# Performance work log

Measured on AMD Instinct MI355X. Metric: run time of the kernel, lower is better.

The kernel has to match this reference:

```python
import jax, jax.numpy as jnp
import numpy as np

B, T_IN, T_OUT = 256, 256, 256
D_IN, HID, OUT = 512, 1024, 1024


def _lstm_step(carry, x_t, W, b):
    # W: [d_x + d_h, 4*d_h] stacked gates (input, forget, output, candidate)
    h, c = carry
    gates = jnp.concatenate([x_t, h], axis=1) @ W + b  # [B, 4*d_h]
    i, f, o, g = jnp.split(gates, 4, axis=1)
    i, f, o = jax.nn.sigmoid(i), jax.nn.sigmoid(f), jax.nn.sigmoid(o)
    g = jnp.tanh(g)
    c_next = f * c + i * g
    h_next = o * jnp.tanh(c_next)
    return (h_next, c_next)


def setup_inputs() -> dict:
    key = jax.random.key(0)
    ks = jax.random.split(key, 9)
    def lin(k, fan_in, fan_out):
        return jax.random.normal(k, (fan_in, fan_out), dtype=jnp.float32) / np.sqrt(fan_in)
    x = jax.random.normal(ks[0], (B, T_IN, D_IN), dtype=jnp.float32)
    enc_W = lin(ks[1], D_IN + HID, 4 * HID)
    enc_b = jnp.zeros((4 * HID,), jnp.float32)
    dec_W = lin(ks[2], HID + OUT, 4 * OUT)
    dec_b = jnp.zeros((4 * OUT,), jnp.float32)
    Wh = lin(ks[3], HID, OUT)
    bh = jnp.zeros((OUT,), jnp.float32)
    Wc = lin(ks[4], HID, OUT)
    bc = jnp.zeros((OUT,), jnp.float32)
    return {"x": x, "enc_W": enc_W, "enc_b": enc_b, "dec_W": dec_W,
            "dec_b": dec_b, "Wh": Wh, "bh": bh, "Wc": Wc, "bc": bc}


def reference(x, enc_W, enc_b, dec_W, dec_b, Wh, bh, Wc, bc):
    Bm = x.shape[0]
    # ---- encoder: scan over time ----
    h0 = jnp.zeros((Bm, HID), x.dtype)
    c0 = jnp.zeros((Bm, HID), x.dtype)
    def enc_step(carry, x_t):
        return _lstm_step(carry, x_t, enc_W, enc_b), None
    (h_enc, c_enc), _ = jax.lax.scan(enc_step, (h0, c0), jnp.swapaxes(x, 0, 1))
    # ---- decoder: constant input = h_enc, init projected states ----
    h_cur = h_enc @ Wh + bh
    c_cur = c_enc @ Wc + bc
    def dec_step(carry, _):
        nxt = _lstm_step(carry, h_enc, dec_W, dec_b)
        return nxt, nxt[0]
    _, hs = jax.lax.scan(dec_step, (h_cur, c_cur), None, length=T_OUT)
    return jnp.swapaxes(hs, 0, 1)  # [B, T_OUT, OUT]
```

## Files before the change

kernel.cpp:

```cpp
#include <hip/hip_runtime.h>
#include <hip/hip_bf16.h>


#define NB   256
#define TSEQ 256
#define DIN  512
#define HID  1024
#define G4   4096

typedef __attribute__((ext_vector_type(8))) __bf16 bf16x8;
typedef __attribute__((ext_vector_type(4))) float  f32x4;

static __device__ __forceinline__ unsigned short f2bf(float v) {
    unsigned u; __builtin_memcpy(&u, &v, 4);
    return (unsigned short)((u + 0x7FFFu + ((u >> 16) & 1u)) >> 16);
}
static __device__ __forceinline__ float bf2f(unsigned short b) {
    unsigned u = ((unsigned)b) << 16; float f; __builtin_memcpy(&f, &u, 4); return f;
}
static __device__ __forceinline__ float fsig(float x) {
    return 1.f / (1.f + __expf(-x));
}
static __device__ __forceinline__ float ftanh(float x) {
    return 2.f / (1.f + __expf(-2.f * x)) - 1.f;
}
template<int AUX>
static __device__ __forceinline__ void glds16(const void* g, void* l) {
    __builtin_amdgcn_global_load_lds(
        (const __attribute__((address_space(1))) unsigned int*)g,
        (__attribute__((address_space(3))) unsigned int*)l, 16, 0, AUX);
}
static __device__ __forceinline__ void st16_ag(unsigned short* p, unsigned short v) {
    asm volatile("global_store_short %0, %1, off sc1"
                 :: "v"(p), "v"((unsigned)v) : "memory");
}
static __device__ __forceinline__ void st32_ag(unsigned* p, unsigned v) {
    asm volatile("global_store_dword %0, %1, off sc1"
                 :: "v"(p), "v"(v) : "memory");
}

__global__ __launch_bounds__(256) void split_transpose(
        const float* __restrict__ W, unsigned short* __restrict__ T_hi,
        unsigned short* __restrict__ T_lo, int K, int N) {
    __shared__ float tile[64][65];
    const int kb = blockIdx.x * 64, nb = blockIdx.y * 64;
    const int tid = threadIdx.x;
    const int r = tid >> 2, c0 = (tid & 3) << 4;
    #pragma unroll
    for (int j = 0; j < 16; j += 4) {
        float4 v = *(const float4*)(W + (size_t)(kb + r) * N + nb + c0 + j);
        tile[r][c0 + j + 0] = v.x; tile[r][c0 + j + 1] = v.y;
        tile[r][c0 + j + 2] = v.z; tile[r][c0 + j + 3] = v.w;
    }
    __syncthreads();
    #pragma unroll
    for (int j = 0; j < 16; ++j) {
        float v = tile[c0 + j][r];
        unsigned short hi = f2bf(v);
        unsigned short lo = f2bf(v - bf2f(hi));
        size_t o = (size_t)(nb + r) * K + kb + c0 + j;
        T_hi[o] = hi; T_lo[o] = lo;
    }
}

__global__ __launch_bounds__(256, 1) void lstm_persist(
        const float* __restrict__ x,
        const unsigned short* __restrict__ encT_hi, const unsigned short* __restrict__ encT_lo,
        const unsigned short* __restrict__ decT_hi, const unsigned short* __restrict__ decT_lo,
        const unsigned short* __restrict__ WhT_hi, const unsigned short* __restrict__ WhT_lo,
        const unsigned short* __restrict__ WcT_hi, const unsigned short* __restrict__ WcT_lo,
        const float* __restrict__ enc_b, const float* __restrict__ dec_b,
        const float* __restrict__ bhv, const float* __restrict__ bcv,
        unsigned short* h_hi0, unsigned short* h_lo0,
        unsigned short* h_hi1, unsigned short* h_lo1,
        unsigned short* ce_hi, unsigned short* ce_lo,
        float* c0, float* c1,
        unsigned short* x_hi0, unsigned short* x_lo0,
        unsigned short* x_hi1, unsigned short* x_lo1,
        unsigned* barcnt, float* __restrict__ out) {
    __shared__ __align__(16) char smem[131072];
    __shared__ float sG[64][68];
    const int wg   = blockIdx.x;
    const int row0 = (wg >> 6) << 6;
    const int hc0  = (wg & 63) << 4;
    const int tid  = threadIdx.x;
    const int lane = tid & 63;
    const int wv   = tid >> 6;
    const int rA   = (wv >> 1) << 5;
    const int cB   = (wv & 1) << 5;
    const int n    = tid & 15, mq = tid >> 4;

    unsigned bar_e = 0;
    auto gbar = [&]() {
        __syncthreads();
        ++bar_e;
        if (tid == 0) {
            __hip_atomic_fetch_add(barcnt + ((wg & 7) << 5), 1u,
                                   __ATOMIC_RELAXED, __HIP_MEMORY_SCOPE_AGENT);
            if (wg == 0) {
                const unsigned target = bar_e << 8;
                for (;;) {
                    unsigned s = 0;
                    #pragma unroll
                    for (int i = 0; i < 8; ++i)
                        s += __hip_atomic_load(barcnt + (i << 5),
                                               __ATOMIC_RELAXED, __HIP_MEMORY_SCOPE_AGENT);
                    if (s >= target) break;
                    __builtin_amdgcn_s_sleep(1);
                }
                __hip_atomic_fetch_add(barcnt + 256, 1u,
                                       __ATOMIC_RELAXED, __HIP_MEMORY_SCOPE_AGENT);
            } else {
                while (__hip_atomic_load(barcnt + 256,
                                         __ATOMIC_RELAXED, __HIP_MEMORY_SCOPE_AGENT) < bar_e)
                    __builtin_amdgcn_s_sleep(2);
            }
        }
        __syncthreads();
    };

    const unsigned short *g_Axh = nullptr, *g_Axl = nullptr;
    const unsigned short *g_Ahh = nullptr, *g_Ahl = nullptr;
    const unsigned short *g_Bh = nullptr, *g_Bl = nullptr;
    int g_sb = 0, g_kb0 = 0, g_nx = 0, g_colw0 = 0, g_arow0 = 0;

    auto stageB = [&](int c, int buf) {
        char* bb = smem + buf * 32768;
        const int k0b = g_kb0 + (c << 6);
        const int kseg = (lane & 7) ^ ((lane >> 3) & 7);
        #pragma unroll
        for (int j = 0; j < 2; ++j) {
            const int colw = g_colw0 + (j << 3) + (lane >> 3);
            const size_t go = (size_t)colw * g_sb + k0b + (kseg << 3);
            const int gclb = (wv << 4) + (j << 3);
            glds16<0>(g_Bh + go, bb + 16384 + (gclb << 7));
            glds16<0>(g_Bl + go, bb + 24576 + (gclb << 7));
        }
    };
    auto stageA = [&](int c, int buf) {
        char* bb = smem + buf * 32768;
        const int kseg = (lane & 7) ^ ((lane >> 3) & 7);
        const unsigned short *Ah, *Al; int sa, ka;
        if (c < g_nx) { Ah = g_Axh; Al = g_Axl; sa = DIN; ka = c << 6; }
        else          { Ah = g_Ahh; Al = g_Ahl; sa = HID; ka = (c - g_nx) << 6; }
        #pragma unroll
        for (int j = 0; j < 2; ++j) {
            const int mb2 = (wv << 4) + (j << 3);
            const int m   = mb2 + (lane >> 3);
            const size_t go = (size_t)(g_arow0 + m) * sa + ka + (kseg << 3);
            glds16<16>(Ah + go, bb + (mb2 << 7));
            glds16<16>(Al + go, bb + 8192 + (mb2 << 7));
        }
    };

    auto compute = [&](const char* bb, f32x4 (&acc)[2][2]) {
        const char* sah = bb;
        const char* sal = bb + 8192;
        const char* sbh = bb + 16384;
        const char* sbl = bb + 24576;
        #pragma unroll
        for (int kk = 0; kk < 2; ++kk) {
            const int kb = (kk << 6) | ((lane >> 4) << 4);
            bf16x8 ah[2], al[2], bh[2], bl[2];
            #pragma unroll
            for (int ms = 0; ms < 2; ++ms) {
                const int m  = rA + (ms << 4) + (lane & 15);
                const int ad = (m << 7) + (kb ^ ((m & 7) << 4));
                ah[ms] = *(const bf16x8*)(sah + ad);
                al[ms] = *(const bf16x8*)(sal + ad);
            }
            #pragma unroll
            for (int ns = 0; ns < 2; ++ns) {
                const int gcl = cB + (ns << 4) + (lane & 15);
                const int ad  = (gcl << 7) + (kb ^ ((gcl & 7) << 4));
                bh[ns] = *(const bf16x8*)(sbh + ad);
                bl[ns] = *(const bf16x8*)(sbl + ad);
            }
            #pragma unroll
            for (int ms = 0; ms < 2; ++ms)
                #pragma unroll
                for (int ns = 0; ns < 2; ++ns) {
                    acc[ms][ns] = __builtin_amdgcn_mfma_f32_16x16x32_bf16(ah[ms], bh[ns], acc[ms][ns], 0, 0, 0);
                    acc[ms][ns] = __builtin_amdgcn_mfma_f32_16x16x32_bf16(al[ms], bh[ns], acc[ms][ns], 0, 0, 0);
                    acc[ms][ns] = __builtin_amdgcn_mfma_f32_16x16x32_bf16(ah[ms], bl[ns], acc[ms][ns], 0, 0, 0);
                }
        }
    };

    auto run_chunks = [&](int nch, f32x4 (&acc)[2][2], int preB) {
        if (!preB) { stageB(0, 0); stageA(0, 0); stageB(1, 1); stageA(1, 1); }
        else       { stageA(0, 0); stageA(1, 1); }
        for (int c = 0; c < nch; ++c) {
            if (c + 2 < nch) {
                stageB(c + 2, (c + 2) & 3);
                stageA(c + 2, (c + 2) & 3);
                if (preB && c == 0)
                    asm volatile("s_waitcnt vmcnt(12)" ::: "memory");
                else
                    asm volatile("s_waitcnt vmcnt(16)" ::: "memory");
            } else if (c + 1 < nch) {
                asm volatile("s_waitcnt vmcnt(8)" ::: "memory");
            } else {
                asm volatile("s_waitcnt vmcnt(0)" ::: "memory");
            }
            __builtin_amdgcn_s_barrier();
            compute(smem + (c & 3) * 32768, acc);
        }
    };

    auto acc2sG = [&](f32x4 (&acc)[2][2]) {
        #pragma unroll
        for (int ms = 0; ms < 2; ++ms)
            #pragma unroll
            for (int ns = 0; ns < 2; ++ns)
                #pragma unroll
                for (int r = 0; r < 4; ++r)
                    sG[cB + (ns << 4) + (lane & 15)]
                      [rA + (ms << 4) + ((lane >> 4) << 2) + r] = acc[ms][ns][r];
    };

    auto convert = [&](int tn) {
        unsigned short* xh = (tn & 1) ? x_hi1 : x_hi0;
        unsigned short* xl = (tn & 1) ? x_lo1 : x_lo0;
        const int r = tid & 63, cp = tid >> 6;
        const int row = row0 + r;
        const int col = ((wg & 63) << 3) + (cp << 1);
        const unsigned long long pv = __builtin_nontemporal_load(
            (const unsigned long long*)(x + ((size_t)row * TSEQ + tn) * DIN + col));
        const float fx = __uint_as_float((unsigned)pv);
        const float fy = __uint_as_float((unsigned)(pv >> 32));
        const unsigned short hx = f2bf(fx), lx = f2bf(fx - bf2f(hx));
        const unsigned short hy = f2bf(fy), ly = f2bf(fy - bf2f(hy));
        st32_ag((unsigned*)(xh + (size_t)row * DIN + col), (unsigned)hx | ((unsigned)hy << 16));
        st32_ag((unsigned*)(xl + (size_t)row * DIN + col), (unsigned)lx | ((unsigned)ly << 16));
    };

    const float be0 = enc_b[hc0 + n];
    const float be1 = enc_b[HID + hc0 + n];
    const float be2 = enc_b[2 * HID + hc0 + n];
    const float be3 = enc_b[3 * HID + hc0 + n];

    g_Bh = encT_hi; g_Bl = encT_lo; g_sb = 1536; g_kb0 = 0; g_nx = 8;
    g_colw0 = wv * HID + hc0; g_arow0 = row0;
    convert(0);
    stageB(0, 0); stageB(1, 1);
    gbar();
    for (int t = 0; t < TSEQ; ++t) {
        g_Axh = (t & 1) ? x_hi1 : x_hi0;  g_Axl = (t & 1) ? x_lo1 : x_lo0;
        g_Ahh = (t & 1) ? h_hi1 : h_hi0;  g_Ahl = (t & 1) ? h_lo1 : h_lo0;
        unsigned short* Ohh = (t & 1) ? h_hi0 : h_hi1;
        unsigned short* Ohl = (t & 1) ? h_lo0 : h_lo1;
        f32x4 acc[2][2];
        { f32x4 z; z[0]=0.f;z[1]=0.f;z[2]=0.f;z[3]=0.f;
          acc[0][0]=z;acc[0][1]=z;acc[1][0]=z;acc[1][1]=z; }
        run_chunks(24, acc, 1);
        acc2sG(acc);
        __syncthreads();
        #pragma unroll
        for (int q = 0; q < 4; ++q) {
            const int m = mq + (q << 4);
            const int grow = row0 + m;
            const float gi = sG[n][m] + be0;
            const float gf = sG[16 + n][m] + be1;
            const float go = sG[32 + n][m] + be2;
            const float gg = sG[48 + n][m] + be3;
            const float si = fsig(gi), sf = fsig(gf), so = fsig(go);
            const float tg = ftanh(gg);
            const size_t ci = (size_t)grow * HID + hc0 + n;
            const float cnew = sf * c0[ci] + si * tg;
            c0[ci] = cnew;
            const float hnew = so * ftanh(cnew);
            const unsigned short hh = f2bf(hnew);
            st16_ag(Ohh + ci, hh);
            st16_ag(Ohl + ci, f2bf(hnew - bf2f(hh)));
            if (t == TSEQ - 1) {
                const unsigned short ch = f2bf(cnew);
                st16_ag(ce_hi + ci, ch);
                st16_ag(ce_lo + ci, f2bf(cnew - bf2f(ch)));
            }
        }
        if (t < TSEQ - 1) {
            convert(t + 1);
            stageB(0, 0); stageB(1, 1);
        }
        gbar();
    }

    float dk[16];
    {
        g_Bh = decT_hi; g_Bl = decT_lo; g_sb = 2048; g_kb0 = 0; g_nx = 0;
        g_Ahh = h_hi0; g_Ahl = h_lo0;
        g_colw0 = wv * HID + hc0; g_arow0 = row0;
        f32x4 acc[2][2];
        { f32x4 z; z[0]=0.f;z[1]=0.f;z[2]=0.f;z[3]=0.f;
          acc[0][0]=z;acc[0][1]=z;acc[1][0]=z;acc[1][1]=z; }
        run_chunks(16, acc, 0);
        acc2sG(acc);
        __syncthreads();
        #pragma unroll
        for (int q = 0; q < 4; ++q) {
            const int m = mq + (q << 4);
            dk[q * 4 + 0] = sG[n][m]      + dec_b[hc0 + n];
            dk[q * 4 + 1] = sG[16 + n][m] + dec_b[HID + hc0 + n];
            dk[q * 4 + 2] = sG[32 + n][m] + dec_b[2 * HID + hc0 + n];
            dk[q * 4 + 3] = sG[48 + n][m] + dec_b[3 * HID + hc0 + n];
        }
        gbar();
    }

    if (wg < 128) {
        const int isWc = wg >> 6;
        const int wgl  = wg & 63;
        const int mgp = wgl >> 4, ngp = wgl & 15;
        g_arow0 = mgp << 6;
        g_colw0 = (ngp << 6) + (wv << 4);
        g_Bh = isWc ? WcT_hi : WhT_hi;  g_Bl = isWc ? WcT_lo : WhT_lo;
        g_sb = 1024; g_kb0 = 0; g_nx = 0;
        g_Ahh = isWc ? ce_hi : h_hi0;   g_Ahl = isWc ? ce_lo : h_lo0;
        f32x4 acc[2][2];
        { f32x4 z; z[0]=0.f;z[1]=0.f;z[2]=0.f;z[3]=0.f;
          acc[0][0]=z;acc[0][1]=z;acc[1][0]=z;acc[1][1]=z; }
        run_chunks(16, acc, 0);
        #pragma unroll
        for (int ms = 0; ms < 2; ++ms)
            #pragma unroll
            for (int ns = 0; ns < 2; ++ns)
                #pragma unroll
                for (int r = 0; r < 4; ++r) {
                    const int rowp = (mgp << 6) + rA + (ms << 4) + ((lane >> 4) << 2) + r;
                    const int colp = (ngp << 6) + cB + (ns << 4) + (lane & 15);
                    const size_t o = (size_t)rowp * HID + colp;
                    if (isWc) {
                        st32_ag((unsigned*)(c1 + o),
                                __float_as_uint(acc[ms][ns][r] + bcv[colp]));
                    } else {
                        const float v = acc[ms][ns][r] + bhv[colp];
                        const unsigned short hh = f2bf(v);
                        st16_ag(h_hi1 + o, hh);
                        st16_ag(h_lo1 + o, f2bf(v - bf2f(hh)));
                    }
                }
    }
    gbar();

    g_Bh = decT_hi; g_Bl = decT_lo; g_sb = 2048; g_kb0 = 1024; g_nx = 0;
    g_colw0 = wv * HID + hc0; g_arow0 = row0;
    float creg[4];
    #pragma unroll
    for (int q = 0; q < 4; ++q) {
        const size_t ci = (size_t)(row0 + mq + (q << 4)) * HID + hc0 + n;
        creg[q] = __uint_as_float(__hip_atomic_load((const unsigned*)(c1 + ci),
                      __ATOMIC_RELAXED, __HIP_MEMORY_SCOPE_AGENT));
    }
    stageB(0, 0); stageB(1, 1);
    for (int t = 0; t < TSEQ; ++t) {
        g_Ahh = (t & 1) ? h_hi0 : h_hi1;  g_Ahl = (t & 1) ? h_lo0 : h_lo1;
        unsigned short* Ohh = (t & 1) ? h_hi1 : h_hi0;
        unsigned short* Ohl = (t & 1) ? h_lo1 : h_lo0;
        f32x4 acc[2][2];
        { f32x4 z; z[0]=0.f;z[1]=0.f;z[2]=0.f;z[3]=0.f;
          acc[0][0]=z;acc[0][1]=z;acc[1][0]=z;acc[1][1]=z; }
        run_chunks(16, acc, 1);
        acc2sG(acc);
        __syncthreads();
        #pragma unroll
        for (int q = 0; q < 4; ++q) {
            const int m = mq + (q << 4);
            const int grow = row0 + m;
            const float gi = sG[n][m]      + dk[q * 4 + 0];
            const float gf = sG[16 + n][m] + dk[q * 4 + 1];
            const float go = sG[32 + n][m] + dk[q * 4 + 2];
            const float gg = sG[48 + n][m] + dk[q * 4 + 3];
            const float si = fsig(gi), sf = fsig(gf), so = fsig(go);
            const float tg = ftanh(gg);
            const float cnew = sf * creg[q] + si * tg;
            creg[q] = cnew;
            const float hnew = so * ftanh(cnew);
            const size_t ci = (size_t)grow * HID + hc0 + n;
            const unsigned short hh = f2bf(hnew);
            st16_ag(Ohh + ci, hh);
            st16_ag(Ohl + ci, f2bf(hnew - bf2f(hh)));
            __builtin_nontemporal_store(hnew,
                out + ((size_t)grow * TSEQ + t) * HID + hc0 + n);
        }
        if (t < TSEQ - 1) {
            stageB(0, 0); stageB(1, 1);
            gbar();
        }
    }
}

extern "C" void kernel_launch(void* const* d_in, const int* in_sizes, int n_in,
                              void* d_out, int out_size, void* d_ws, size_t ws_size,
                              hipStream_t stream) {
    (void)in_sizes; (void)n_in; (void)out_size;
    const float* x     = (const float*)d_in[0];
    const float* enc_W = (const float*)d_in[1];
    const float* enc_b = (const float*)d_in[2];
    const float* dec_W = (const float*)d_in[3];
    const float* dec_b = (const float*)d_in[4];
    const float* Wh    = (const float*)d_in[5];
    const float* bh    = (const float*)d_in[6];
    const float* Wc    = (const float*)d_in[7];
    const float* bc    = (const float*)d_in[8];
    float* out = (float*)d_out;

    char* w = (char*)d_ws;
    size_t off = 0;
    auto alloc = [&](size_t bytes) -> void* {
        off = (off + 255) & ~(size_t)255;
        void* p = w + off;
        off += bytes;
        return p;
    };
    unsigned short* encT_hi = (unsigned short*)alloc((size_t)G4 * 1536 * 2);
    unsigned short* encT_lo = (unsigned short*)alloc((size_t)G4 * 1536 * 2);
    unsigned short* decT_hi = (unsigned short*)alloc((size_t)G4 * 2048 * 2);
    unsigned short* decT_lo = (unsigned short*)alloc((size_t)G4 * 2048 * 2);
    unsigned short* WhT_hi  = (unsigned short*)alloc((size_t)HID * HID * 2);
    unsigned short* WhT_lo  = (unsigned short*)alloc((size_t)HID * HID * 2);
    unsigned short* WcT_hi  = (unsigned short*)alloc((size_t)HID * HID * 2);
    unsigned short* WcT_lo  = (unsigned short*)alloc((size_t)HID * HID * 2);
    unsigned short* h_hi0 = (unsigned short*)alloc((size_t)NB * HID * 2);
    unsigned short* h_lo0 = (unsigned short*)alloc((size_t)NB * HID * 2);
    unsigned short* h_hi1 = (unsigned short*)alloc((size_t)NB * HID * 2);
    unsigned short* h_lo1 = (unsigned short*)alloc((size_t)NB * HID * 2);
    unsigned short* ce_hi = (unsigned short*)alloc((size_t)NB * HID * 2);
    unsigned short* ce_lo = (unsigned short*)alloc((size_t)NB * HID * 2);
    float* c0 = (float*)alloc((size_t)NB * HID * 4);
    float* c1 = (float*)alloc((size_t)NB * HID * 4);
    unsigned short* x_hi0 = (unsigned short*)alloc((size_t)NB * DIN * 2);
    unsigned short* x_lo0 = (unsigned short*)alloc((size_t)NB * DIN * 2);
    unsigned short* x_hi1 = (unsigned short*)alloc((size_t)NB * DIN * 2);
    unsigned short* x_lo1 = (unsigned short*)alloc((size_t)NB * DIN * 2);
    unsigned* barcnt = (unsigned*)alloc(2048);
    if (off > ws_size) return;

    split_transpose<<<dim3(1536 / 64, G4 / 64), 256, 0, stream>>>(enc_W, encT_hi, encT_lo, 1536, G4);
    split_transpose<<<dim3(2048 / 64, G4 / 64), 256, 0, stream>>>(dec_W, decT_hi, decT_lo, 2048, G4);
    split_transpose<<<dim3(HID / 64, HID / 64), 256, 0, stream>>>(Wh, WhT_hi, WhT_lo, HID, HID);
    split_transpose<<<dim3(HID / 64, HID / 64), 256, 0, stream>>>(Wc, WcT_hi, WcT_lo, HID, HID);
    (void)hipMemsetAsync(h_hi0, 0, (size_t)NB * HID * 2, stream);
    (void)hipMemsetAsync(h_lo0, 0, (size_t)NB * HID * 2, stream);
    (void)hipMemsetAsync(c0,    0, (size_t)NB * HID * 4, stream);
    (void)hipMemsetAsync(barcnt, 0, 2048, stream);

    lstm_persist<<<256, 256, 0, stream>>>(
        x, encT_hi, encT_lo, decT_hi, decT_lo, WhT_hi, WhT_lo, WcT_hi, WcT_lo,
        enc_b, dec_b, bh, bc,
        h_hi0, h_lo0, h_hi1, h_lo1, ce_hi, ce_lo, c0, c1,
        x_hi0, x_lo0, x_hi1, x_lo1, barcnt, out);
}
```

Baseline: 10.59 ms.

## Load A operand via registers with deeper prefetch pipeline instead of direct-to-LDS

```diff
diff --git a/kernel.cpp b/kernel.cpp
--- a/kernel.cpp
+++ b/kernel.cpp
@@ -10,6 +10,9 @@
 
 typedef __attribute__((ext_vector_type(8))) __bf16 bf16x8;
 typedef __attribute__((ext_vector_type(4))) float  f32x4;
+typedef unsigned long long ull;
+
+struct alignas(16) ull2 { ull a, b; };
 
 static __device__ __forceinline__ unsigned short f2bf(float v) {
     unsigned u; __builtin_memcpy(&u, &v, 4);
@@ -24,11 +27,10 @@
 static __device__ __forceinline__ float ftanh(float x) {
     return 2.f / (1.f + __expf(-2.f * x)) - 1.f;
 }
-template<int AUX>
 static __device__ __forceinline__ void glds16(const void* g, void* l) {
     __builtin_amdgcn_global_load_lds(
         (const __attribute__((address_space(1))) unsigned int*)g,
-        (__attribute__((address_space(3))) unsigned int*)l, 16, 0, AUX);
+        (__attribute__((address_space(3))) unsigned int*)l, 16, 0, 0);
 }
 static __device__ __forceinline__ void st16_ag(unsigned short* p, unsigned short v) {
     asm volatile("global_store_short %0, %1, off sc1"
@@ -78,7 +80,7 @@
         unsigned short* x_hi0, unsigned short* x_lo0,
         unsigned short* x_hi1, unsigned short* x_lo1,
         unsigned* barcnt, float* __restrict__ out) {
-    __shared__ __align__(16) char smem[131072];
+    __shared__ __align__(16) char smem[98304];
     __shared__ float sG[64][68];
     const int wg   = blockIdx.x;
     const int row0 = (wg >> 6) << 6;
@@ -125,7 +127,7 @@
     int g_sb = 0, g_kb0 = 0, g_nx = 0, g_colw0 = 0, g_arow0 = 0;
 
     auto stageB = [&](int c, int buf) {
-        char* bb = smem + buf * 32768;
+        char* bb = smem + 32768 + buf * 16384;
         const int k0b = g_kb0 + (c << 6);
         const int kseg = (lane & 7) ^ ((lane >> 3) & 7);
         #pragma unroll
@@ -133,31 +135,44 @@
             const int colw = g_colw0 + (j << 3) + (lane >> 3);
             const size_t go = (size_t)colw * g_sb + k0b + (kseg << 3);
             const int gclb = (wv << 4) + (j << 3);
-            glds16<0>(g_Bh + go, bb + 16384 + (gclb << 7));
-            glds16<0>(g_Bl + go, bb + 24576 + (gclb << 7));
-        }
-    };
-    auto stageA = [&](int c, int buf) {
-        char* bb = smem + buf * 32768;
-        const int kseg = (lane & 7) ^ ((lane >> 3) & 7);
+            glds16(g_Bh + go, bb + (gclb << 7));
+            glds16(g_Bl + go, bb + 8192 + (gclb << 7));
+        }
+    };
+
+    auto aload = [&](int ch, ull (&r)[8]) {
         const unsigned short *Ah, *Al; int sa, ka;
-        if (c < g_nx) { Ah = g_Axh; Al = g_Axl; sa = DIN; ka = c << 6; }
-        else          { Ah = g_Ahh; Al = g_Ahl; sa = HID; ka = (c - g_nx) << 6; }
-        #pragma unroll
-        for (int j = 0; j < 2; ++j) {
-            const int mb2 = (wv << 4) + (j << 3);
-            const int m   = mb2 + (lane >> 3);
-            const size_t go = (size_t)(g_arow0 + m) * sa + ka + (kseg << 3);
-            glds16<16>(Ah + go, bb + (mb2 << 7));
-            glds16<16>(Al + go, bb + 8192 + (mb2 << 7));
-        }
-    };
-
-    auto compute = [&](const char* bb, f32x4 (&acc)[2][2]) {
-        const char* sah = bb;
-        const char* sal = bb + 8192;
-        const char* sbh = bb + 16384;
-        const char* sbl = bb + 24576;
+        if (ch < g_nx) { Ah = g_Axh; Al = g_Axl; sa = DIN; ka = ch << 6; }
+        else           { Ah = g_Ahh; Al = g_Ahl; sa = HID; ka = (ch - g_nx) << 6; }
+        const int qa = tid & 3, mA = tid >> 2;
+        const ull* ph = (const ull*)(Ah + (size_t)(g_arow0 + mA) * sa + ka + (qa << 4));
+        const ull* pl = (const ull*)(Al + (size_t)(g_arow0 + mA) * sa + ka + (qa << 4));
+        #pragma unroll
+        for (int i = 0; i < 4; ++i)
+            r[i] = __hip_atomic_load(ph + i, __ATOMIC_RELAXED, __HIP_MEMORY_SCOPE_AGENT);
+        #pragma unroll
+        for (int i = 0; i < 4; ++i)
+            r[4 + i] = __hip_atomic_load(pl + i, __ATOMIC_RELAXED, __HIP_MEMORY_SCOPE_AGENT);
+    };
+    auto dswrite = [&](int ch, const ull (&r)[8]) {
+        char* ab = smem + (ch & 1) * 16384;
+        const int qa = tid & 3, mA = tid >> 2;
+        const int base = mA << 7, sw = mA & 7;
+        const int o0 = base + ((((qa << 1) + 0) ^ sw) << 4);
+        const int o1 = base + ((((qa << 1) + 1) ^ sw) << 4);
+        *(ull2*)(ab + o0)        = ull2{r[0], r[1]};
+        *(ull2*)(ab + o1)        = ull2{r[2], r[3]};
+        *(ull2*)(ab + 8192 + o0) = ull2{r[4], r[5]};
+        *(ull2*)(ab + 8192 + o1) = ull2{r[6], r[7]};
+    };
+
+    auto compute = [&](int c, f32x4 (&acc)[2][2]) {
+        const char* ab  = smem + (c & 1) * 16384;
+        const char* bbf = smem + 32768 + (c & 3) * 16384;
+        const char* sah = ab;
+        const char* sal = ab + 8192;
+        const char* sbh = bbf;
+        const char* sbl = bbf + 8192;
         #pragma unroll
         for (int kk = 0; kk < 2; ++kk) {
             const int kb = (kk << 6) | ((lane >> 4) << 4);
@@ -187,24 +202,43 @@
         }
     };
 
-    auto run_chunks = [&](int nch, f32x4 (&acc)[2][2], int preB) {
-        if (!preB) { stageB(0, 0); stageA(0, 0); stageB(1, 1); stageA(1, 1); }
-        else       { stageA(0, 0); stageA(1, 1); }
-        for (int c = 0; c < nch; ++c) {
-            if (c + 2 < nch) {
-                stageB(c + 2, (c + 2) & 3);
-                stageA(c + 2, (c + 2) & 3);
-                if (preB && c == 0)
-                    asm volatile("s_waitcnt vmcnt(12)" ::: "memory");
-                else
-                    asm volatile("s_waitcnt vmcnt(16)" ::: "memory");
-            } else if (c + 1 < nch) {
-                asm volatile("s_waitcnt vmcnt(8)" ::: "memory");
-            } else {
-                asm volatile("s_waitcnt vmcnt(0)" ::: "memory");
-            }
-            __builtin_amdgcn_s_barrier();
-            compute(smem + (c & 3) * 32768, acc);
+    auto vwait = [&](int nw) {
+        if (nw >= 32)      asm volatile("s_waitcnt vmcnt(32)" ::: "memory");
+        else if (nw == 24) asm volatile("s_waitcnt vmcnt(24)" ::: "memory");
+        else if (nw == 16) asm volatile("s_waitcnt vmcnt(16)" ::: "memory");
+        else if (nw == 4)  asm volatile("s_waitcnt vmcnt(4)"  ::: "memory");
+        else               asm volatile("s_waitcnt vmcnt(0)"  ::: "memory");
+    };
+
+    auto body = [&](int c, int nch, ull (&sw)[8], f32x4 (&acc)[2][2]) {
+        int nw;
+        if (c == 0) nw = 16;
+        else if (c == 1) nw = 24;
+        else {
+            const int rem = nch - 1 - c;
+            nw = (rem >= 4) ? 32 : (rem == 3) ? 24 : (rem == 2) ? 16 : (rem == 1) ? 4 : 0;
+        }
+        vwait(nw);
+        asm volatile("s_waitcnt lgkmcnt(0)" ::: "memory");
+        __builtin_amdgcn_s_barrier();
+        if (c + 1 < nch) dswrite(c + 1, sw);
+        if (c + 3 < nch) stageB(c + 3, (c + 3) & 3);
+        if (c + 5 < nch) aload(c + 5, sw);
+        compute(c, acc);
+    };
+
+    auto run_chunks = [&](int nch, f32x4 (&acc)[2][2]) {
+        ull r0[8], r1[8], r2[8], r3[8];
+        aload(0, r0); aload(1, r1); aload(2, r2); aload(3, r3);
+        stageB(0, 0); stageB(1, 1); stageB(2, 2);
+        asm volatile("s_waitcnt vmcnt(36)" ::: "memory");
+        dswrite(0, r0);
+        aload(4, r0);
+        for (int cb = 0; cb < nch; cb += 4) {
+            body(cb + 0, nch, r1, acc);
+            body(cb + 1, nch, r2, acc);
+            body(cb + 2, nch, r3, acc);
+            body(cb + 3, nch, r0, acc);
         }
     };
 
@@ -225,8 +259,8 @@
         const int r = tid & 63, cp = tid >> 6;
         const int row = row0 + r;
         const int col = ((wg & 63) << 3) + (cp << 1);
-        const unsigned long long pv = __builtin_nontemporal_load(
-            (const unsigned long long*)(x + ((size_t)row * TSEQ + tn) * DIN + col));
+        const ull pv = __builtin_nontemporal_load(
+            (const ull*)(x + ((size_t)row * TSEQ + tn) * DIN + col));
         const float fx = __uint_as_float((unsigned)pv);
         const float fy = __uint_as_float((unsigned)(pv >> 32));
         const unsigned short hx = f2bf(fx), lx = f2bf(fx - bf2f(hx));
@@ -243,7 +277,6 @@
     g_Bh = encT_hi; g_Bl = encT_lo; g_sb = 1536; g_kb0 = 0; g_nx = 8;
     g_colw0 = wv * HID + hc0; g_arow0 = row0;
     convert(0);
-    stageB(0, 0); stageB(1, 1);
     gbar();
     for (int t = 0; t < TSEQ; ++t) {
         g_Axh = (t & 1) ? x_hi1 : x_hi0;  g_Axl = (t & 1) ? x_lo1 : x_lo0;
@@ -253,7 +286,7 @@
         f32x4 acc[2][2];
         { f32x4 z; z[0]=0.f;z[1]=0.f;z[2]=0.f;z[3]=0.f;
           acc[0][0]=z;acc[0][1]=z;acc[1][0]=z;acc[1][1]=z; }
-        run_chunks(24, acc, 1);
+        run_chunks(24, acc);
         acc2sG(acc);
         __syncthreads();
         #pragma unroll
@@ -279,10 +312,7 @@
                 st16_ag(ce_lo + ci, f2bf(cnew - bf2f(ch)));
             }
         }
-        if (t < TSEQ - 1) {
-            convert(t + 1);
-            stageB(0, 0); stageB(1, 1);
-        }
+        if (t < TSEQ - 1) convert(t + 1);
         gbar();
     }
 
@@ -294,7 +324,7 @@
         f32x4 acc[2][2];
         { f32x4 z; z[0]=0.f;z[1]=0.f;z[2]=0.f;z[3]=0.f;
           acc[0][0]=z;acc[0][1]=z;acc[1][0]=z;acc[1][1]=z; }
-        run_chunks(16, acc, 0);
+        run_chunks(16, acc);
         acc2sG(acc);
         __syncthreads();
         #pragma unroll
@@ -320,7 +350,7 @@
         f32x4 acc[2][2];
         { f32x4 z; z[0]=0.f;z[1]=0.f;z[2]=0.f;z[3]=0.f;
           acc[0][0]=z;acc[0][1]=z;acc[1][0]=z;acc[1][1]=z; }
-        run_chunks(16, acc, 0);
+        run_chunks(16, acc);
         #pragma unroll
         for (int ms = 0; ms < 2; ++ms)
             #pragma unroll
@@ -352,7 +382,7 @@
         creg[q] = __uint_as_float(__hip_atomic_load((const unsigned*)(c1 + ci),
                       __ATOMIC_RELAXED, __HIP_MEMORY_SCOPE_AGENT));
     }
-    stageB(0, 0); stageB(1, 1);
+    asm volatile("s_waitcnt vmcnt(0)" ::: "memory");
     for (int t = 0; t < TSEQ; ++t) {
         g_Ahh = (t & 1) ? h_hi0 : h_hi1;  g_Ahl = (t & 1) ? h_lo0 : h_lo1;
         unsigned short* Ohh = (t & 1) ? h_hi1 : h_hi0;
@@ -360,7 +390,7 @@
         f32x4 acc[2][2];
         { f32x4 z; z[0]=0.f;z[1]=0.f;z[2]=0.f;z[3]=0.f;
           acc[0][0]=z;acc[0][1]=z;acc[1][0]=z;acc[1][1]=z; }
-        run_chunks(16, acc, 1);
+        run_chunks(16, acc);
         acc2sG(acc);
         __syncthreads();
         #pragma unroll
@@ -383,10 +413,7 @@
             __builtin_nontemporal_store(hnew,
                 out + ((size_t)grow * TSEQ + t) * HID + hc0 + n);
         }
-        if (t < TSEQ - 1) {
-            stageB(0, 0); stageB(1, 1);
-            gbar();
-        }
+        if (t < TSEQ - 1) gbar();
     }
 }
 
```

After: 15.39 ms. 1.45x slower.
